# Performance work log

Hardware: AMD Instinct MI355X
Metric: run time of the kernel (lower is better)

## Reference

```python
import jax, jax.numpy as jnp
import numpy as np

K = 3        # kernel_size
S = 1        # stride
PAD = 1      # padding
BITS = 8
MAX_VAL = 2.5
DELTA = MAX_VAL / (2 ** (BITS - 1) - 1)


def im2col(x, k, s, p):
    # x: [N, C, H, W] -> cols: [N, C*k*k, h_out*w_out] (same layout as F.unfold)
    n, c, h, w = x.shape
    h_out = (h - k + 2 * p) // s + 1
    w_out = (w - k + 2 * p) // s + 1
    xp = jnp.pad(x, ((0, 0), (0, 0), (p, p), (p, p)))
    patches = jnp.stack(
        [xp[:, :, i : i + (h_out - 1) * s + 1 : s, j : j + (w_out - 1) * s + 1 : s]
         for i in range(k) for j in range(k)],
        axis=2,
    )  # [N, C, k*k, h_out, w_out]
    return patches.reshape(n, c * k * k, h_out * w_out), h_out, w_out


def setup_inputs() -> dict:
    key = jax.random.key(0)
    k1, k2 = jax.random.split(key)
    x = jax.random.normal(k1, (8, 64, 32, 32), dtype=jnp.float32)
    W = jax.random.normal(k2, (64, 64, 3, 3), dtype=jnp.float32)  # adder parameter
    return {"x": x, "W": W}


def reference(x, W):
    # Inference path: needs_input_grad[0] is False, so weights are NOT quantized.
    n = x.shape[0]
    n_filters = W.shape[0]
    cols, h_out, w_out = im2col(x, K, S, PAD)              # [N, CKK, L]
    X_col = jnp.transpose(cols, (1, 2, 0)).reshape(cols.shape[1], -1)  # [CKK, L*N]
    W_col = W.reshape(n_filters, -1)                        # [F, CKK]
    # Stream over filters to avoid the [F, CKK, P] broadcast blowup.
    out = jax.lax.map(lambda w: -jnp.abs(w[:, None] - X_col).sum(0), W_col)  # [F, P]
    out = out.reshape(n_filters, h_out, w_out, n)
    return jnp.transpose(out, (3, 0, 1, 2))  # [N, F, h_out, w_out]
```

## Files before the change

### kernel.cpp

```cpp
#include <hip/hip_runtime.h>
#include <stdint.h>


typedef _Float16 half2v __attribute__((ext_vector_type(2)));

#define XS   20
#define RH   18
#define CH2  32
#define XCHW (RH * XS)
#define W2_U32 (CH2 * 16 * 9 * 4)
#define WS_NEEDED (W2_U32 * 4 + 64 * 4)

__global__ __launch_bounds__(64)
void prep_kernel(const float* __restrict__ W, uint32_t* __restrict__ W2,
                 float* __restrict__ SW) {
    const int f    = blockIdx.x;
    const int lane = threadIdx.x;
    float s = 0.0f;
    for (int i = lane; i < CH2 * 9; i += 64) {
        const int ch2 = i / 9;
        const int k   = i - ch2 * 9;
        const float a = W[(size_t)f * 576 + (2 * ch2) * 9 + k];
        const float b = W[(size_t)f * 576 + (2 * ch2 + 1) * 9 + k];
        const _Float16 ha = (_Float16)a;
        const _Float16 hb = (_Float16)b;
        const uint16_t ua = __builtin_bit_cast(uint16_t, ha);
        const uint16_t ub = __builtin_bit_cast(uint16_t, hb);
        W2[((((size_t)ch2 * 16 + (f >> 2)) * 9 + k) << 2) + (f & 3)] =
            (uint32_t)ua | ((uint32_t)ub << 16);
        s += (float)ha + (float)hb;
    }
#pragma unroll
    for (int m = 32; m >= 1; m >>= 1) s += __shfl_xor(s, m, 64);
    if (lane == 0) SW[f] = s;
}

__global__ __launch_bounds__(512, 2)
void adder2d_kernel(const float* __restrict__ x,
                    const uint4* __restrict__ W2,
                    const float* __restrict__ SW,
                    float* __restrict__ out) {
    __shared__ uint32_t xs[CH2 * XCHW];
    __shared__ uint4 wl[CH2 * 9];

    const int bid     = blockIdx.x;
    const int quarter = bid & 3;
    const int fg      = (bid >> 2) & 15;
    const int n       = bid >> 6;
    const int r0      = (quarter >> 1) * 16;
    const int c0      = (quarter & 1) * 16;
    const int tid     = threadIdx.x;

    for (int idx = tid; idx < CH2 * 9; idx += 512) {
        const int ch2 = idx / 9;
        const int k   = idx - 9 * ch2;
        wl[idx] = W2[((size_t)ch2 * 16 + fg) * 9 + k];
    }

    {
        const int ch2s = tid >> 4;
        const int sub  = tid & 15;
        const float* xa = x + ((size_t)n * 64 + 2 * ch2s) * 1024;
        for (int cell = sub; cell < RH * RH; cell += 16) {
            const int row = cell / RH;
            const int col = cell - row * RH;
            const int ir  = r0 + row - 1;
            const int ic  = c0 + col - 1;
            float a = 0.0f, b = 0.0f;
            if ((unsigned)ir < 32u && (unsigned)ic < 32u) {
                a = xa[ir * 32 + ic];
                b = xa[1024 + ir * 32 + ic];
            }
            const _Float16 ha = (_Float16)a;
            const _Float16 hb = (_Float16)b;
            xs[ch2s * XCHW + row * XS + col] =
                (uint32_t)__builtin_bit_cast(uint16_t, ha) |
                ((uint32_t)__builtin_bit_cast(uint16_t, hb) << 16);
        }
    }
    __syncthreads();

    const int wave = __builtin_amdgcn_readfirstlane(tid >> 6);
    const int lane = tid & 63;
    const int tx   = lane & 7;
    const int ty   = lane >> 3;

    const half2v one2 = {(_Float16)1.0f, (_Float16)1.0f};
    float acc[16];
    float sx[4];
#pragma unroll
    for (int i = 0; i < 16; ++i) acc[i] = 0.0f;
#pragma unroll
    for (int i = 0; i < 4; ++i) sx[i] = 0.0f;

#pragma unroll
    for (int i = 0; i < 4; ++i) {
        const int ch2 = wave * 4 + i;

        uint32_t xw[4][4];
#pragma unroll
        for (int r = 0; r < 4; ++r) {
            const uint32_t* p = &xs[ch2 * XCHW + (2 * ty + r) * XS + 2 * tx];
            const uint2 A = *(const uint2*)p;
            const uint2 B = *(const uint2*)(p + 2);
            xw[r][0] = A.x; xw[r][1] = A.y; xw[r][2] = B.x; xw[r][3] = B.y;
        }

#pragma unroll
        for (int k = 0; k < 9; ++k) {
            const int ki = k / 3, kj = k - 3 * ki;
            const uint4 wk = wl[ch2 * 9 + k];
            const uint32_t wf_[4] = {wk.x, wk.y, wk.z, wk.w};
#pragma unroll
            for (int sr = 0; sr < 2; ++sr)
#pragma unroll
                for (int sc = 0; sc < 2; ++sc) {
                    const half2v xv =
                        __builtin_bit_cast(half2v, xw[sr + ki][sc + kj]);
                    const int sub = sr * 2 + sc;
                    sx[sub] = __builtin_amdgcn_fdot2(xv, one2, sx[sub], false);
#pragma unroll
                    for (int f = 0; f < 4; ++f) {
                        const half2v w2 = __builtin_bit_cast(half2v, wf_[f]);
                        const half2v m  = __builtin_elementwise_min(w2, xv);
                        acc[f * 4 + sub] =
                            __builtin_amdgcn_fdot2(m, one2, acc[f * 4 + sub], false);
                    }
                }
        }
    }

    __syncthreads();
    float* ps = (float*)xs;
#pragma unroll
    for (int s = 0; s < 16; ++s) ps[((wave * 64 + lane) * 20) + s] = acc[s];
#pragma unroll
    for (int s = 0; s < 4; ++s) ps[((wave * 64 + lane) * 20) + 16 + s] = sx[s];
    __syncthreads();

    const int px  = tid & 255;
    const int fp  = tid >> 8;
    const int row = px >> 4, col = px & 15;
    const int lane_s = (row >> 1) * 8 + (col >> 1);
    const int sub_s  = (row & 1) * 2 + (col & 1);

    float sxs = 0.0f;
#pragma unroll
    for (int w = 0; w < 8; ++w)
        sxs += ps[(w * 64 + lane_s) * 20 + 16 + sub_s];
#pragma unroll
    for (int f2 = 0; f2 < 2; ++f2) {
        const int f = fp * 2 + f2;
        float m = 0.0f;
#pragma unroll
        for (int w = 0; w < 8; ++w)
            m += ps[(w * 64 + lane_s) * 20 + f * 4 + sub_s];
        const float val = 2.0f * m - SW[fg * 4 + f] - sxs;
        out[(((size_t)n * 64 + fg * 4 + f) * 32 + r0 + row) * 32 + c0 + col] = val;
    }
}

#define FB_CCHUNK 16
#define FB_XROW 36
#define FB_XCH (10 * FB_XROW)
#define FB_WPAD 12
__global__ __launch_bounds__(256, 6)
void adder2d_fb(const float* __restrict__ x, const float* __restrict__ Wt,
                float* __restrict__ out) {
    __shared__ float fxs[FB_CCHUNK * FB_XCH];
    __shared__ float fws[4 * FB_CCHUNK * FB_WPAD];
    const int bid = blockIdx.x;
    const int ks = bid & 3, fg = (bid >> 2) & 15, tile = (bid >> 6) & 3, n = bid >> 8;
    const int c0 = ks * FB_CCHUNK, f0 = fg * 4, i0 = tile * 8, tid = threadIdx.x;
    for (int idx = tid; idx < 4 * FB_CCHUNK * 9; idx += 256) {
        const int f = idx / (FB_CCHUNK * 9), rem = idx - f * (FB_CCHUNK * 9);
        const int cc = rem / 9, kk = rem - cc * 9;
        fws[(f * FB_CCHUNK + cc) * FB_WPAD + kk] =
            Wt[((size_t)(f0 + f) * 64 + (c0 + cc)) * 9 + kk];
    }
    const float* xn = x + ((size_t)n * 64 + c0) * 1024;
    for (int idx = tid; idx < FB_CCHUNK * FB_XCH; idx += 256) {
        const int cc = idx / FB_XCH, rem = idx - cc * FB_XCH;
        const int row = rem / FB_XROW, col = rem - row * FB_XROW;
        const int ir = i0 + row - 1, ic = col - 1;
        float v = 0.0f;
        if ((unsigned)ir < 32u && (unsigned)ic < 32u) v = xn[cc * 1024 + ir * 32 + ic];
        fxs[idx] = v;
    }
    __syncthreads();
    const int r = tid >> 5, j = tid & 31;
    float acc[4] = {0, 0, 0, 0};
#pragma unroll 2
    for (int cc = 0; cc < FB_CCHUNK; ++cc) {
        const float* xp = &fxs[cc * FB_XCH + r * FB_XROW + j];
        const float x00 = xp[0], x01 = xp[1], x02 = xp[2];
        const float x10 = xp[36], x11 = xp[37], x12 = xp[38];
        const float x20 = xp[72], x21 = xp[73], x22 = xp[74];
#pragma unroll
        for (int f = 0; f < 4; ++f) {
            const float* wq = &fws[(f * FB_CCHUNK + cc) * FB_WPAD];
            acc[f] += fabsf(wq[0] - x00) + fabsf(wq[1] - x01) + fabsf(wq[2] - x02)
                    + fabsf(wq[3] - x10) + fabsf(wq[4] - x11) + fabsf(wq[5] - x12)
                    + fabsf(wq[6] - x20) + fabsf(wq[7] - x21) + fabsf(wq[8] - x22);
        }
    }
    const int irow = i0 + r;
#pragma unroll
    for (int f = 0; f < 4; ++f)
        atomicAdd(&out[(((size_t)n * 64 + (f0 + f)) * 32 + irow) * 32 + j], -acc[f]);
}

extern "C" void kernel_launch(void* const* d_in, const int* in_sizes, int n_in,
                              void* d_out, int out_size, void* d_ws, size_t ws_size,
                              hipStream_t stream) {
    const float* x  = (const float*)d_in[0];
    const float* W  = (const float*)d_in[1];
    float* out      = (float*)d_out;

    if (ws_size >= (size_t)WS_NEEDED) {
        uint32_t* W2 = (uint32_t*)d_ws;
        float* SW    = (float*)((char*)d_ws + (size_t)W2_U32 * 4);
        hipLaunchKernelGGL(prep_kernel, dim3(64), dim3(64), 0, stream, W, W2, SW);
        hipLaunchKernelGGL(adder2d_kernel, dim3(512), dim3(512), 0, stream,
                           x, (const uint4*)W2, SW, out);
    } else {
        hipMemsetAsync(d_out, 0, (size_t)out_size * sizeof(float), stream);
        hipLaunchKernelGGL(adder2d_fb, dim3(2048), dim3(256), 0, stream, x, W, out);
    }
}
```

Baseline: 80.55 us.

## Pre-pack fp16 input tiles in prep kernel and accumulate with packed half adds

The prep kernel now also converts x into padded fp16-pair tiles in workspace, one per (image, quarter), so the main kernel only does a straight uint4 copy into LDS instead of 16 redundant conversions per tile across filter groups. The inner loop accumulates min and x sums as packed half2 adds rather than fdot2 into fp32, which halves the accumulation instruction cost per element. The fp16 accumulation over 36 terms per lane loses precision compared with fp32, and the prep kernel now runs only 48 blocks of mostly serial conversion work. The workspace requirement also grows, so the fast path is skipped when the workspace is too small.

```diff
diff --git a/kernel.cpp b/kernel.cpp
--- a/kernel.cpp
+++ b/kernel.cpp
@@ -8,39 +8,73 @@
 #define RH   18
 #define CH2  32
 #define XCHW (RH * XS)
-#define W2_U32 (CH2 * 16 * 9 * 4)
-#define WS_NEEDED (W2_U32 * 4 + 64 * 4)
-
-__global__ __launch_bounds__(64)
-void prep_kernel(const float* __restrict__ W, uint32_t* __restrict__ W2,
-                 float* __restrict__ SW) {
-    const int f    = blockIdx.x;
-    const int lane = threadIdx.x;
-    float s = 0.0f;
-    for (int i = lane; i < CH2 * 9; i += 64) {
-        const int ch2 = i / 9;
-        const int k   = i - ch2 * 9;
-        const float a = W[(size_t)f * 576 + (2 * ch2) * 9 + k];
-        const float b = W[(size_t)f * 576 + (2 * ch2 + 1) * 9 + k];
-        const _Float16 ha = (_Float16)a;
-        const _Float16 hb = (_Float16)b;
-        const uint16_t ua = __builtin_bit_cast(uint16_t, ha);
-        const uint16_t ub = __builtin_bit_cast(uint16_t, hb);
-        W2[((((size_t)ch2 * 16 + (f >> 2)) * 9 + k) << 2) + (f & 3)] =
-            (uint32_t)ua | ((uint32_t)ub << 16);
-        s += (float)ha + (float)hb;
-    }
-#pragma unroll
-    for (int m = 32; m >= 1; m >>= 1) s += __shfl_xor(s, m, 64);
-    if (lane == 0) SW[f] = s;
+#define TILE_U32 (CH2 * XCHW)
+#define W2_U32   (CH2 * 16 * 9 * 4)
+#define XP_U32   (8 * 4 * TILE_U32)
+#define WS_NEEDED ((size_t)(W2_U32 + 64 + XP_U32) * 4)
+
+__device__ inline float h2sum(uint32_t u) {
+    const half2v h = __builtin_bit_cast(half2v, u);
+    return (float)h.x + (float)h.y;
+}
+
+__global__ __launch_bounds__(256)
+void prep_kernel(const float* __restrict__ x, const float* __restrict__ W,
+                 uint32_t* __restrict__ W2, float* __restrict__ SW,
+                 uint32_t* __restrict__ Xp) {
+    const int b   = blockIdx.x;
+    const int tid = threadIdx.x;
+    if (b < 16) {
+        const int f    = b * 4 + (tid >> 6);
+        const int lane = tid & 63;
+        float s = 0.0f;
+        for (int i = lane; i < CH2 * 9; i += 64) {
+            const int ch2 = i / 9;
+            const int k   = i - ch2 * 9;
+            const _Float16 ha = (_Float16)W[(size_t)f * 576 + (2 * ch2) * 9 + k];
+            const _Float16 hb = (_Float16)W[(size_t)f * 576 + (2 * ch2 + 1) * 9 + k];
+            W2[((((size_t)ch2 * 16 + (f >> 2)) * 9 + k) << 2) + (f & 3)] =
+                (uint32_t)__builtin_bit_cast(uint16_t, ha) |
+                ((uint32_t)__builtin_bit_cast(uint16_t, hb) << 16);
+            s += (float)ha + (float)hb;
+        }
+#pragma unroll
+        for (int m = 32; m >= 1; m >>= 1) s += __shfl_xor(s, m, 64);
+        if (lane == 0) SW[f] = s;
+    } else {
+        const int b2 = b - 16;
+        const int n  = b2 >> 2;
+        const int q  = b2 & 3;
+        const int r0 = (q >> 1) * 16;
+        const int c0 = (q & 1) * 16;
+        uint32_t* dst = Xp + (size_t)b2 * TILE_U32;
+        const float* xn = x + (size_t)n * 64 * 1024;
+        for (int i = tid; i < TILE_U32; i += 256) {
+            const int ch2 = i / XCHW;
+            const int rem = i - ch2 * XCHW;
+            const int row = rem / XS;
+            const int col = rem - row * XS;
+            const int ir  = r0 + row - 1;
+            const int ic  = c0 + col - 1;
+            float a = 0.0f, bb = 0.0f;
+            if ((unsigned)ir < 32u && (unsigned)ic < 32u) {
+                a  = xn[(size_t)(2 * ch2) * 1024 + ir * 32 + ic];
+                bb = xn[(size_t)(2 * ch2 + 1) * 1024 + ir * 32 + ic];
+            }
+            const _Float16 ha = (_Float16)a;
+            const _Float16 hb = (_Float16)bb;
+            dst[i] = (uint32_t)__builtin_bit_cast(uint16_t, ha) |
+                     ((uint32_t)__builtin_bit_cast(uint16_t, hb) << 16);
+        }
+    }
 }
 
 __global__ __launch_bounds__(512, 2)
-void adder2d_kernel(const float* __restrict__ x,
+void adder2d_kernel(const uint32_t* __restrict__ Xp,
                     const uint4* __restrict__ W2,
                     const float* __restrict__ SW,
                     float* __restrict__ out) {
-    __shared__ uint32_t xs[CH2 * XCHW];
+    __shared__ uint32_t xs[TILE_U32];
     __shared__ uint4 wl[CH2 * 9];
 
     const int bid     = blockIdx.x;
@@ -51,32 +85,20 @@
     const int c0      = (quarter & 1) * 16;
     const int tid     = threadIdx.x;
 
-    for (int idx = tid; idx < CH2 * 9; idx += 512) {
-        const int ch2 = idx / 9;
-        const int k   = idx - 9 * ch2;
-        wl[idx] = W2[((size_t)ch2 * 16 + fg) * 9 + k];
+    if (tid < CH2 * 9) {
+        const int ch2 = tid / 9;
+        const int k   = tid - 9 * ch2;
+        wl[tid] = W2[((size_t)ch2 * 16 + fg) * 9 + k];
     }
 
     {
-        const int ch2s = tid >> 4;
-        const int sub  = tid & 15;
-        const float* xa = x + ((size_t)n * 64 + 2 * ch2s) * 1024;
-        for (int cell = sub; cell < RH * RH; cell += 16) {
-            const int row = cell / RH;
-            const int col = cell - row * RH;
-            const int ir  = r0 + row - 1;
-            const int ic  = c0 + col - 1;
-            float a = 0.0f, b = 0.0f;
-            if ((unsigned)ir < 32u && (unsigned)ic < 32u) {
-                a = xa[ir * 32 + ic];
-                b = xa[1024 + ir * 32 + ic];
-            }
-            const _Float16 ha = (_Float16)a;
-            const _Float16 hb = (_Float16)b;
-            xs[ch2s * XCHW + row * XS + col] =
-                (uint32_t)__builtin_bit_cast(uint16_t, ha) |
-                ((uint32_t)__builtin_bit_cast(uint16_t, hb) << 16);
-        }
+        const uint4* src = (const uint4*)(Xp + (size_t)(n * 4 + quarter) * TILE_U32);
+        uint4* dst = (uint4*)xs;
+#pragma unroll
+        for (int it = 0; it < 5; ++it)
+            dst[it * 512 + tid] = src[it * 512 + tid];
+        if (tid < (TILE_U32 / 4 - 2560))
+            dst[2560 + tid] = src[2560 + tid];
     }
     __syncthreads();
 
@@ -85,13 +107,12 @@
     const int tx   = lane & 7;
     const int ty   = lane >> 3;
 
-    const half2v one2 = {(_Float16)1.0f, (_Float16)1.0f};
-    float acc[16];
-    float sx[4];
-#pragma unroll
-    for (int i = 0; i < 16; ++i) acc[i] = 0.0f;
-#pragma unroll
-    for (int i = 0; i < 4; ++i) sx[i] = 0.0f;
+    half2v acc[16];
+    half2v sx[4];
+#pragma unroll
+    for (int i = 0; i < 16; ++i) acc[i] = (half2v){(_Float16)0.f, (_Float16)0.f};
+#pragma unroll
+    for (int i = 0; i < 4; ++i) sx[i] = (half2v){(_Float16)0.f, (_Float16)0.f};
 
 #pragma unroll
     for (int i = 0; i < 4; ++i) {
@@ -118,24 +139,25 @@
                     const half2v xv =
                         __builtin_bit_cast(half2v, xw[sr + ki][sc + kj]);
                     const int sub = sr * 2 + sc;
-                    sx[sub] = __builtin_amdgcn_fdot2(xv, one2, sx[sub], false);
+                    sx[sub] = sx[sub] + xv;
 #pragma unroll
                     for (int f = 0; f < 4; ++f) {
                         const half2v w2 = __builtin_bit_cast(half2v, wf_[f]);
-                        const half2v m  = __builtin_elementwise_min(w2, xv);
-                        acc[f * 4 + sub] =
-                            __builtin_amdgcn_fdot2(m, one2, acc[f * 4 + sub], false);
+                        acc[f * 4 + sub] = acc[f * 4 + sub] +
+                            __builtin_elementwise_min(w2, xv);
                     }
                 }
         }
     }
 
     __syncthreads();
-    float* ps = (float*)xs;
-#pragma unroll
-    for (int s = 0; s < 16; ++s) ps[((wave * 64 + lane) * 20) + s] = acc[s];
-#pragma unroll
-    for (int s = 0; s < 4; ++s) ps[((wave * 64 + lane) * 20) + 16 + s] = sx[s];
+    uint32_t* ps = xs;
+#pragma unroll
+    for (int s = 0; s < 16; ++s)
+        ps[(wave * 64 + lane) * 20 + s] = __builtin_bit_cast(uint32_t, acc[s]);
+#pragma unroll
+    for (int s = 0; s < 4; ++s)
+        ps[(wave * 64 + lane) * 20 + 16 + s] = __builtin_bit_cast(uint32_t, sx[s]);
     __syncthreads();
 
     const int px  = tid & 255;
@@ -147,14 +169,14 @@
     float sxs = 0.0f;
 #pragma unroll
     for (int w = 0; w < 8; ++w)
-        sxs += ps[(w * 64 + lane_s) * 20 + 16 + sub_s];
+        sxs += h2sum(ps[(w * 64 + lane_s) * 20 + 16 + sub_s]);
 #pragma unroll
     for (int f2 = 0; f2 < 2; ++f2) {
         const int f = fp * 2 + f2;
         float m = 0.0f;
 #pragma unroll
         for (int w = 0; w < 8; ++w)
-            m += ps[(w * 64 + lane_s) * 20 + f * 4 + sub_s];
+            m += h2sum(ps[(w * 64 + lane_s) * 20 + f * 4 + sub_s]);
         const float val = 2.0f * m - SW[fg * 4 + f] - sxs;
         out[(((size_t)n * 64 + fg * 4 + f) * 32 + r0 + row) * 32 + c0 + col] = val;
     }
@@ -217,12 +239,14 @@
     const float* W  = (const float*)d_in[1];
     float* out      = (float*)d_out;
 
-    if (ws_size >= (size_t)WS_NEEDED) {
+    if (ws_size >= WS_NEEDED) {
         uint32_t* W2 = (uint32_t*)d_ws;
         float* SW    = (float*)((char*)d_ws + (size_t)W2_U32 * 4);
-        hipLaunchKernelGGL(prep_kernel, dim3(64), dim3(64), 0, stream, W, W2, SW);
+        uint32_t* Xp = (uint32_t*)((char*)d_ws + (size_t)(W2_U32 + 64) * 4);
+        hipLaunchKernelGGL(prep_kernel, dim3(48), dim3(256), 0, stream,
+                           x, W, W2, SW, Xp);
         hipLaunchKernelGGL(adder2d_kernel, dim3(512), dim3(512), 0, stream,
-                           x, (const uint4*)W2, SW, out);
+                           Xp, (const uint4*)W2, SW, out);
     } else {
         hipMemsetAsync(d_out, 0, (size_t)out_size * sizeof(float), stream);
         hipLaunchKernelGGL(adder2d_fb, dim3(2048), dim3(256), 0, stream, x, W, out);
```

Result: slower. 88.21 us (+9.5%).
